# Kernel tuning notes

Measured on AMD Instinct MI355X. Metric: run time of the kernel, lower is better.

## Reference

```python
import jax, jax.numpy as jnp
import numpy as np
import math

HEAD_DEPTH = 16
CLIP = 10.0
NEG_INF = 1.0e10
# combined scale: (1/sqrt(head_depth)) * log_50(400)
SCALE = (math.log(400.0) / math.log(50.0)) / math.sqrt(HEAD_DEPTH)


def setup_inputs() -> dict:
    key = jax.random.key(0)
    kq, kk, kv, km = jax.random.split(key, 4)
    B, H, S, D = 4, 8, 2048, HEAD_DEPTH
    Q = jax.random.normal(kq, (B, H, S, D), dtype=jnp.float32)
    K = jax.random.normal(kk, (B, H, S, D), dtype=jnp.float32)
    V = jax.random.normal(kv, (B, H, S, D), dtype=jnp.float32)
    # mask: (B, n_nodes, 1) bool; True -> masked (logit set to -inf)
    mask = jax.random.randint(km, (B, S, 1), 0, 2) == 1
    return {"Q": Q, "K": K, "V": V, "mask": mask}


def reference(Q, K, V, mask):
    # logits: (B, H, q_seq, k_seq)
    logits = jnp.einsum("bhqd,bhkd->bhqk", Q, K) * SCALE
    logits = CLIP * jnp.tanh(logits)  # tanh clip
    # mask[:, None, None, :, 0] -> (B, 1, 1, k_seq), True gets -inf
    m = mask[:, None, None, :, 0]
    logits = jnp.where(m, -NEG_INF, logits)
    probs = jax.nn.softmax(logits, axis=-1)
    return jnp.einsum("bhqk,bhkd->bhqd", probs, V)
```

## Files before the change

kernel.cpp:

```cpp
#include <hip/hip_runtime.h>


typedef __fp16 h2 __attribute__((ext_vector_type(2)));
typedef __fp16 h4 __attribute__((ext_vector_type(4)));
typedef float  f4 __attribute__((ext_vector_type(4)));
typedef unsigned short us4 __attribute__((ext_vector_type(4)));

#define SEQ 2048

__device__ __forceinline__ float fast_exp2(float x) {
#if __has_builtin(__builtin_amdgcn_exp2f)
    return __builtin_amdgcn_exp2f(x);
#else
    return exp2f(x);
#endif
}

__device__ __forceinline__ float dot2acc(h2 a, float accv) {
#if __has_builtin(__builtin_amdgcn_fdot2)
    const h2 one = {(__fp16)1.0f, (__fp16)1.0f};
    return __builtin_amdgcn_fdot2(a, one, accv, false);
#else
    return accv + (float)a[0] + (float)a[1];
#endif
}

__global__ __launch_bounds__(512, 8) void attn_fused(
    const float* __restrict__ Qp, const float* __restrict__ Kp,
    const float* __restrict__ Vp, const int* __restrict__ maskp,
    float* __restrict__ out)
{
    __shared__ __align__(16) _Float16 Kbuf[2][4096];
    __shared__ __align__(16) _Float16 Vbuf[2][4096];
    __shared__ __align__(16) unsigned short idx16[SEQ];
    __shared__ int wsum[8];

    const int bid  = blockIdx.x;
    const int bh   = bid >> 5;
    const int qblk = bid & 31;
    const int b    = bh >> 3;
    const int tid  = threadIdx.x;
    const int wave = tid >> 6;
    const int lane = tid & 63;
    const int qt   = wave & 3;
    const int kg   = wave >> 2;
    const int c    = lane & 15;
    const int g    = lane >> 4;

    const size_t base  = (size_t)bh * (SEQ * 16);
    const int    qbase = qblk * 64 + qt * 16;
    const float  c1 = 1.1047809f;
    const float  c2 = -28.8539008f;

    h4 qfrag;
    {
        f4 qv = *(const f4*)(Qp + base + (size_t)(qbase + c) * 16 + 4 * g);
        h2 lo = __builtin_amdgcn_cvt_pkrtz(c1 * qv[0], c1 * qv[1]);
        h2 hi = __builtin_amdgcn_cvt_pkrtz(c1 * qv[2], c1 * qv[3]);
        qfrag[0] = lo[0]; qfrag[1] = lo[1]; qfrag[2] = hi[0]; qfrag[3] = hi[1];
    }

    int4 mv = *(const int4*)(maskp + (size_t)b * SEQ + tid * 4);
    const int k0 = (mv.x == 0), k1 = (mv.y == 0),
              k2 = (mv.z == 0), k3 = (mv.w == 0);
    const int cnt4 = k0 + k1 + k2 + k3;
    int inc = cnt4;
    #pragma unroll
    for (int off = 1; off < 64; off <<= 1) {
        int v = __shfl_up(inc, off);
        if (lane >= off) inc += v;
    }
    *(us4*)&idx16[tid * 4] = (us4){0, 0, 0, 0};
    if (lane == 63) wsum[wave] = inc;
    __syncthreads();
    int tot = 0, wpre = 0;
    #pragma unroll
    for (int w = 0; w < 8; ++w) {
        int s = wsum[w];
        if (w < wave) wpre += s;
        tot += s;
    }
    int pos = wpre + inc - cnt4;
    if (k0) idx16[pos++] = (unsigned short)(tid * 4 + 0);
    if (k1) idx16[pos++] = (unsigned short)(tid * 4 + 1);
    if (k2) idx16[pos++] = (unsigned short)(tid * 4 + 2);
    if (k3) idx16[pos++] = (unsigned short)(tid * 4 + 3);
    __syncthreads();

    int nr = (tot + 255) >> 8;
    if (nr == 0) nr = 1;

    const int u  = tid & 31;
    const int tt = tid >> 5;
    const int gc = u & 15;
    const int gh = u >> 4;

    const float* Kb = Kp + base;
    const float* Vb = Vp + base;

    const int fs0 = (tt * 64 + u)      * 4;
    const int fs1 = (tt * 64 + u + 32) * 4;

    f4 kA, kB;
    float vA0, vA1, vA2, vA3, vB0, vB1, vB2, vB3;

    {
        us4 ra = *(const us4*)&idx16[tt * 16 + 4 * gh];
        us4 rb = *(const us4*)&idx16[tt * 16 + 4 * gh + 8];
        const int krow = idx16[tt * 16 + gc];
        const float* kr = Kb + (size_t)krow * 16;
        f4 ka_ = *(const f4*)(kr + 4 * gh);
        f4 kb_ = *(const f4*)(kr + 4 * gh + 8);
        float a0 = Vb[(size_t)ra[0] * 16 + gc];
        float a1 = Vb[(size_t)ra[1] * 16 + gc];
        float a2 = Vb[(size_t)ra[2] * 16 + gc];
        float a3 = Vb[(size_t)ra[3] * 16 + gc];
        float b0 = Vb[(size_t)rb[0] * 16 + gc];
        float b1 = Vb[(size_t)rb[1] * 16 + gc];
        float b2 = Vb[(size_t)rb[2] * 16 + gc];
        float b3 = Vb[(size_t)rb[3] * 16 + gc];
        h2 x0 = __builtin_amdgcn_cvt_pkrtz(ka_[0], ka_[1]);
        h2 x1 = __builtin_amdgcn_cvt_pkrtz(ka_[2], ka_[3]);
        h4 kha; kha[0] = x0[0]; kha[1] = x0[1]; kha[2] = x1[0]; kha[3] = x1[1];
        *(h4*)&Kbuf[0][fs0] = kha;
        h2 y0 = __builtin_amdgcn_cvt_pkrtz(kb_[0], kb_[1]);
        h2 y1 = __builtin_amdgcn_cvt_pkrtz(kb_[2], kb_[3]);
        h4 khb; khb[0] = y0[0]; khb[1] = y0[1]; khb[2] = y1[0]; khb[3] = y1[1];
        *(h4*)&Kbuf[0][fs1] = khb;
        h2 p0 = __builtin_amdgcn_cvt_pkrtz(a0, a1);
        h2 p1 = __builtin_amdgcn_cvt_pkrtz(a2, a3);
        h4 vha; vha[0] = p0[0]; vha[1] = p0[1]; vha[2] = p1[0]; vha[3] = p1[1];
        *(h4*)&Vbuf[0][fs0] = vha;
        h2 q0 = __builtin_amdgcn_cvt_pkrtz(b0, b1);
        h2 q1 = __builtin_amdgcn_cvt_pkrtz(b2, b3);
        h4 vhb; vhb[0] = q0[0]; vhb[1] = q0[1]; vhb[2] = q1[0]; vhb[3] = q1[1];
        *(h4*)&Vbuf[0][fs1] = vhb;
    }
    {
        const int r1 = (nr > 1) ? 1 : 0;
        const int ib = r1 * 256 + tt * 16;
        us4 ra = *(const us4*)&idx16[ib + 4 * gh];
        us4 rb = *(const us4*)&idx16[ib + 4 * gh + 8];
        const int krow = idx16[ib + gc];
        const float* kr = Kb + (size_t)krow * 16;
        kA = *(const f4*)(kr + 4 * gh);
        kB = *(const f4*)(kr + 4 * gh + 8);
        vA0 = Vb[(size_t)ra[0] * 16 + gc];
        vA1 = Vb[(size_t)ra[1] * 16 + gc];
        vA2 = Vb[(size_t)ra[2] * 16 + gc];
        vA3 = Vb[(size_t)ra[3] * 16 + gc];
        vB0 = Vb[(size_t)rb[0] * 16 + gc];
        vB1 = Vb[(size_t)rb[1] * 16 + gc];
        vB2 = Vb[(size_t)rb[2] * 16 + gc];
        vB3 = Vb[(size_t)rb[3] * 16 + gc];
    }
    __syncthreads();

    f4 acc = {0.f, 0.f, 0.f, 0.f};
    float dsum = 0.f;

    for (int r = 0; r < nr; ++r) {
        const int cb = r & 1, nb = cb ^ 1;
        if (r + 1 < nr) {
            h2 x0 = __builtin_amdgcn_cvt_pkrtz(kA[0], kA[1]);
            h2 x1 = __builtin_amdgcn_cvt_pkrtz(kA[2], kA[3]);
            h4 kha; kha[0] = x0[0]; kha[1] = x0[1]; kha[2] = x1[0]; kha[3] = x1[1];
            *(h4*)&Kbuf[nb][fs0] = kha;
            h2 y0 = __builtin_amdgcn_cvt_pkrtz(kB[0], kB[1]);
            h2 y1 = __builtin_amdgcn_cvt_pkrtz(kB[2], kB[3]);
            h4 khb; khb[0] = y0[0]; khb[1] = y0[1]; khb[2] = y1[0]; khb[3] = y1[1];
            *(h4*)&Kbuf[nb][fs1] = khb;
            h2 p0 = __builtin_amdgcn_cvt_pkrtz(vA0, vA1);
            h2 p1 = __builtin_amdgcn_cvt_pkrtz(vA2, vA3);
            h4 vha; vha[0] = p0[0]; vha[1] = p0[1]; vha[2] = p1[0]; vha[3] = p1[1];
            *(h4*)&Vbuf[nb][fs0] = vha;
            h2 q0 = __builtin_amdgcn_cvt_pkrtz(vB0, vB1);
            h2 q1 = __builtin_amdgcn_cvt_pkrtz(vB2, vB3);
            h4 vhb; vhb[0] = q0[0]; vhb[1] = q0[1]; vhb[2] = q1[0]; vhb[3] = q1[1];
            *(h4*)&Vbuf[nb][fs1] = vhb;
        }
        if (r + 2 < nr) {
            const int ib = (r + 2) * 256 + tt * 16;
            us4 ra = *(const us4*)&idx16[ib + 4 * gh];
            us4 rb = *(const us4*)&idx16[ib + 4 * gh + 8];
            const int krow = idx16[ib + gc];
            const float* kr = Kb + (size_t)krow * 16;
            kA = *(const f4*)(kr + 4 * gh);
            kB = *(const f4*)(kr + 4 * gh + 8);
            vA0 = Vb[(size_t)ra[0] * 16 + gc];
            vA1 = Vb[(size_t)ra[1] * 16 + gc];
            vA2 = Vb[(size_t)ra[2] * 16 + gc];
            vA3 = Vb[(size_t)ra[3] * 16 + gc];
            vB0 = Vb[(size_t)rb[0] * 16 + gc];
            vB1 = Vb[(size_t)rb[1] * 16 + gc];
            vB2 = Vb[(size_t)rb[2] * 16 + gc];
            vB3 = Vb[(size_t)rb[3] * 16 + gc];
        }

        const _Float16* Kc = &Kbuf[cb][kg * 2048];
        const _Float16* Vc = &Vbuf[cb][kg * 2048];
        const int lim = tot - r * 256 - kg * 128 - 4 * g;

        #pragma unroll
        for (int t = 0; t < 8; ++t) {
            h4 afrag = *(const h4*)(Kc + t * 256 + lane * 4);
            f4 s = __builtin_amdgcn_mfma_f32_16x16x16f16(
                afrag, qfrag, (f4){0.f, 0.f, 0.f, 0.f}, 0, 0, 0);

            float p[4];
            #pragma unroll
            for (int i = 0; i < 4; ++i) {
                float tv = fast_exp2(s[i]);
                float w  = __builtin_amdgcn_rcpf(1.0f + tv);
                float bsel = (t * 16 + i < lim) ? 0.0f : -1.0e30f;
                p[i] = fast_exp2(__builtin_fmaf(c2, w, bsel));
            }
            h2 plo = __builtin_amdgcn_cvt_pkrtz(p[0], p[1]);
            h2 phi = __builtin_amdgcn_cvt_pkrtz(p[2], p[3]);
            dsum = dot2acc(plo, dsum);
            dsum = dot2acc(phi, dsum);
            h4 pf; pf[0] = plo[0]; pf[1] = plo[1]; pf[2] = phi[0]; pf[3] = phi[1];

            h4 vfrag = *(const h4*)(Vc + t * 256 + lane * 4);
            acc = __builtin_amdgcn_mfma_f32_16x16x16f16(pf, vfrag, acc, 0, 0, 0);
        }
        __syncthreads();
    }

    dsum += __shfl_xor(dsum, 16);
    dsum += __shfl_xor(dsum, 32);

    float* ex = (float*)&Kbuf[0][0];
    const int slot = (qt * 64 + lane) * 5;
    if (kg == 1) {
        ex[slot + 0] = acc[0]; ex[slot + 1] = acc[1];
        ex[slot + 2] = acc[2]; ex[slot + 3] = acc[3];
        ex[slot + 4] = dsum;
    }
    __syncthreads();
    if (kg == 0) {
        const float dT = dsum + ex[slot + 4];
        #pragma unroll
        for (int i = 0; i < 4; ++i) {
            const float denom = __shfl(dT, 4 * g + i);
            out[base + (size_t)(qbase + 4 * g + i) * 16 + c] =
                (acc[i] + ex[slot + i]) / denom;
        }
    }
}

extern "C" void kernel_launch(void* const* d_in, const int* in_sizes, int n_in,
                              void* d_out, int out_size, void* d_ws, size_t ws_size,
                              hipStream_t stream) {
    const float* Q    = (const float*)d_in[0];
    const float* K    = (const float*)d_in[1];
    const float* V    = (const float*)d_in[2];
    const int*   mask = (const int*)d_in[3];
    float* out = (float*)d_out;
    attn_fused<<<dim3(1024), dim3(512), 0, stream>>>(Q, K, V, mask, out);
}
```

Baseline: 94.12 us.

## Process two query tiles per wave, halve grid, skip masking on full chunks

Each wave now computes two 16-row query tiles against the same shared K/V fragments. This halves the number of blocks and the total gather/convert work for compacted K/V per query. Full chunks drop the per-element mask-select computation, and the final partial chunk iterates only over the tiles that are populated. The trade-offs are more registers per thread (launch bounds relaxed to 4), fewer blocks in flight on the device, and a longer serial dependency chain per wave.

```diff
diff --git a/kernel.cpp b/kernel.cpp
--- a/kernel.cpp
+++ b/kernel.cpp
@@ -25,7 +25,23 @@
 #endif
 }
 
-__global__ __launch_bounds__(512, 8) void attn_fused(
+__device__ __forceinline__ h4 prob4(f4 s, f4 bsel, float c2, float& dsum) {
+    float p[4];
+    #pragma unroll
+    for (int i = 0; i < 4; ++i) {
+        float tv = fast_exp2(s[i]);
+        float w  = __builtin_amdgcn_rcpf(1.0f + tv);
+        p[i] = fast_exp2(__builtin_fmaf(c2, w, bsel[i]));
+    }
+    h2 plo = __builtin_amdgcn_cvt_pkrtz(p[0], p[1]);
+    h2 phi = __builtin_amdgcn_cvt_pkrtz(p[2], p[3]);
+    dsum = dot2acc(plo, dsum);
+    dsum = dot2acc(phi, dsum);
+    h4 pf; pf[0] = plo[0]; pf[1] = plo[1]; pf[2] = phi[0]; pf[3] = phi[1];
+    return pf;
+}
+
+__global__ __launch_bounds__(512, 4) void attn_fused(
     const float* __restrict__ Qp, const float* __restrict__ Kp,
     const float* __restrict__ Vp, const int* __restrict__ maskp,
     float* __restrict__ out)
@@ -36,8 +52,8 @@
     __shared__ int wsum[8];
 
     const int bid  = blockIdx.x;
-    const int bh   = bid >> 5;
-    const int qblk = bid & 31;
+    const int bh   = bid >> 4;
+    const int qblk = bid & 15;
     const int b    = bh >> 3;
     const int tid  = threadIdx.x;
     const int wave = tid >> 6;
@@ -48,16 +64,21 @@
     const int g    = lane >> 4;
 
     const size_t base  = (size_t)bh * (SEQ * 16);
-    const int    qbase = qblk * 64 + qt * 16;
+    const int    qb0   = qblk * 128 + qt * 16;
+    const int    qb1   = qb0 + 64;
     const float  c1 = 1.1047809f;
     const float  c2 = -28.8539008f;
 
-    h4 qfrag;
+    h4 qfrag0, qfrag1;
     {
-        f4 qv = *(const f4*)(Qp + base + (size_t)(qbase + c) * 16 + 4 * g);
+        f4 qv = *(const f4*)(Qp + base + (size_t)(qb0 + c) * 16 + 4 * g);
         h2 lo = __builtin_amdgcn_cvt_pkrtz(c1 * qv[0], c1 * qv[1]);
         h2 hi = __builtin_amdgcn_cvt_pkrtz(c1 * qv[2], c1 * qv[3]);
-        qfrag[0] = lo[0]; qfrag[1] = lo[1]; qfrag[2] = hi[0]; qfrag[3] = hi[1];
+        qfrag0[0] = lo[0]; qfrag0[1] = lo[1]; qfrag0[2] = hi[0]; qfrag0[3] = hi[1];
+        f4 qw = *(const f4*)(Qp + base + (size_t)(qb1 + c) * 16 + 4 * g);
+        h2 l2 = __builtin_amdgcn_cvt_pkrtz(c1 * qw[0], c1 * qw[1]);
+        h2 h2_ = __builtin_amdgcn_cvt_pkrtz(c1 * qw[2], c1 * qw[3]);
+        qfrag1[0] = l2[0]; qfrag1[1] = l2[1]; qfrag1[2] = h2_[0]; qfrag1[3] = h2_[1];
     }
 
     int4 mv = *(const int4*)(maskp + (size_t)b * SEQ + tid * 4);
@@ -156,8 +177,8 @@
     }
     __syncthreads();
 
-    f4 acc = {0.f, 0.f, 0.f, 0.f};
-    float dsum = 0.f;
+    f4 acc0 = {0.f, 0.f, 0.f, 0.f}, acc1 = {0.f, 0.f, 0.f, 0.f};
+    float dsum0 = 0.f, dsum1 = 0.f;
 
     for (int r = 0; r < nr; ++r) {
         const int cb = r & 1, nb = cb ^ 1;
@@ -199,52 +220,75 @@
 
         const _Float16* Kc = &Kbuf[cb][kg * 2048];
         const _Float16* Vc = &Vbuf[cb][kg * 2048];
-        const int lim = tot - r * 256 - kg * 128 - 4 * g;
-
-        #pragma unroll
-        for (int t = 0; t < 8; ++t) {
-            h4 afrag = *(const h4*)(Kc + t * 256 + lane * 4);
-            f4 s = __builtin_amdgcn_mfma_f32_16x16x16f16(
-                afrag, qfrag, (f4){0.f, 0.f, 0.f, 0.f}, 0, 0, 0);
-
-            float p[4];
+
+        if (r + 1 < nr) {
+            const f4 z = {0.f, 0.f, 0.f, 0.f};
             #pragma unroll
-            for (int i = 0; i < 4; ++i) {
-                float tv = fast_exp2(s[i]);
-                float w  = __builtin_amdgcn_rcpf(1.0f + tv);
-                float bsel = (t * 16 + i < lim) ? 0.0f : -1.0e30f;
-                p[i] = fast_exp2(__builtin_fmaf(c2, w, bsel));
+            for (int t = 0; t < 8; ++t) {
+                h4 afrag = *(const h4*)(Kc + t * 256 + lane * 4);
+                f4 s0 = __builtin_amdgcn_mfma_f32_16x16x16f16(
+                    afrag, qfrag0, (f4){0.f, 0.f, 0.f, 0.f}, 0, 0, 0);
+                f4 s1 = __builtin_amdgcn_mfma_f32_16x16x16f16(
+                    afrag, qfrag1, (f4){0.f, 0.f, 0.f, 0.f}, 0, 0, 0);
+                h4 pf0 = prob4(s0, z, c2, dsum0);
+                h4 pf1 = prob4(s1, z, c2, dsum1);
+                h4 vfrag = *(const h4*)(Vc + t * 256 + lane * 4);
+                acc0 = __builtin_amdgcn_mfma_f32_16x16x16f16(pf0, vfrag, acc0, 0, 0, 0);
+                acc1 = __builtin_amdgcn_mfma_f32_16x16x16f16(pf1, vfrag, acc1, 0, 0, 0);
             }
-            h2 plo = __builtin_amdgcn_cvt_pkrtz(p[0], p[1]);
-            h2 phi = __builtin_amdgcn_cvt_pkrtz(p[2], p[3]);
-            dsum = dot2acc(plo, dsum);
-            dsum = dot2acc(phi, dsum);
-            h4 pf; pf[0] = plo[0]; pf[1] = plo[1]; pf[2] = phi[0]; pf[3] = phi[1];
-
-            h4 vfrag = *(const h4*)(Vc + t * 256 + lane * 4);
-            acc = __builtin_amdgcn_mfma_f32_16x16x16f16(pf, vfrag, acc, 0, 0, 0);
+        } else {
+            const int rem  = tot - r * 256 - kg * 128;
+            int tcnt = (rem <= 0) ? 0 : ((rem + 15) >> 4);
+            if (tcnt > 8) tcnt = 8;
+            const int lim = rem - 4 * g;
+            for (int t = 0; t < tcnt; ++t) {
+                h4 afrag = *(const h4*)(Kc + t * 256 + lane * 4);
+                f4 s0 = __builtin_amdgcn_mfma_f32_16x16x16f16(
+                    afrag, qfrag0, (f4){0.f, 0.f, 0.f, 0.f}, 0, 0, 0);
+                f4 s1 = __builtin_amdgcn_mfma_f32_16x16x16f16(
+                    afrag, qfrag1, (f4){0.f, 0.f, 0.f, 0.f}, 0, 0, 0);
+                f4 bsel;
+                #pragma unroll
+                for (int i = 0; i < 4; ++i)
+                    bsel[i] = (t * 16 + i < lim) ? 0.0f : -1.0e30f;
+                h4 pf0 = prob4(s0, bsel, c2, dsum0);
+                h4 pf1 = prob4(s1, bsel, c2, dsum1);
+                h4 vfrag = *(const h4*)(Vc + t * 256 + lane * 4);
+                acc0 = __builtin_amdgcn_mfma_f32_16x16x16f16(pf0, vfrag, acc0, 0, 0, 0);
+                acc1 = __builtin_amdgcn_mfma_f32_16x16x16f16(pf1, vfrag, acc1, 0, 0, 0);
+            }
         }
         __syncthreads();
     }
 
-    dsum += __shfl_xor(dsum, 16);
-    dsum += __shfl_xor(dsum, 32);
+    dsum0 += __shfl_xor(dsum0, 16);
+    dsum0 += __shfl_xor(dsum0, 32);
+    dsum1 += __shfl_xor(dsum1, 16);
+    dsum1 += __shfl_xor(dsum1, 32);
 
     float* ex = (float*)&Kbuf[0][0];
-    const int slot = (qt * 64 + lane) * 5;
+    const int slot0 = ((qt)     * 64 + lane) * 5;
+    const int slot1 = ((qt + 4) * 64 + lane) * 5;
     if (kg == 1) {
-        ex[slot + 0] = acc[0]; ex[slot + 1] = acc[1];
-        ex[slot + 2] = acc[2]; ex[slot + 3] = acc[3];
-        ex[slot + 4] = dsum;
+        ex[slot0 + 0] = acc0[0]; ex[slot0 + 1] = acc0[1];
+        ex[slot0 + 2] = acc0[2]; ex[slot0 + 3] = acc0[3];
+        ex[slot0 + 4] = dsum0;
+        ex[slot1 + 0] = acc1[0]; ex[slot1 + 1] = acc1[1];
+        ex[slot1 + 2] = acc1[2]; ex[slot1 + 3] = acc1[3];
+        ex[slot1 + 4] = dsum1;
     }
     __syncthreads();
     if (kg == 0) {
-        const float dT = dsum + ex[slot + 4];
+        const float dT0 = dsum0 + ex[slot0 + 4];
+        const float dT1 = dsum1 + ex[slot1 + 4];
         #pragma unroll
         for (int i = 0; i < 4; ++i) {
-            const float denom = __shfl(dT, 4 * g + i);
-            out[base + (size_t)(qbase + 4 * g + i) * 16 + c] =
-                (acc[i] + ex[slot + i]) / denom;
+            const float den0 = __shfl(dT0, 4 * g + i);
+            out[base + (size_t)(qb0 + 4 * g + i) * 16 + c] =
+                (acc0[i] + ex[slot0 + i]) / den0;
+            const float den1 = __shfl(dT1, 4 * g + i);
+            out[base + (size_t)(qb1 + 4 * g + i) * 16 + c] =
+                (acc1[i] + ex[slot1 + i]) / den1;
         }
     }
 }
@@ -257,5 +301,5 @@
     const float* V    = (const float*)d_in[2];
     const int*   mask = (const int*)d_in[3];
     float* out = (float*)d_out;
-    attn_fused<<<dim3(1024), dim3(512), 0, stream>>>(Q, K, V, mask, out);
-}
+    attn_fused<<<dim3(512), dim3(512), 0, stream>>>(Q, K, V, mask, out);
+}
```

After: 91.03 us, median of 2. -3.3%, faster.

## Process four query tiles per block to reuse staged K/V and skip masked tail

Applied to the files above, without the earlier changes.

Each block now handles 256 queries (four 16-row Q fragments per wave) instead of 64, so every gathered and fp16-converted K/V tile in shared memory is reused across four times as many queries and the grid shrinks from 1024 to 256 blocks. The last round is split into its own path that only iterates over tiles holding valid (unmasked) keys and applies the mask bias there, while full rounds skip the mask select. This cuts global gather traffic and conversion work per query, at the cost of more registers per thread, a lower occupancy hint, and only 256 blocks, which may leave compute units underused.

```diff
diff --git a/kernel.cpp b/kernel.cpp
--- a/kernel.cpp
+++ b/kernel.cpp
@@ -25,7 +25,23 @@
 #endif
 }
 
-__global__ __launch_bounds__(512, 8) void attn_fused(
+__device__ __forceinline__ h4 prob4(f4 s, f4 bsel, float c2, float& dsum) {
+    float p[4];
+    #pragma unroll
+    for (int i = 0; i < 4; ++i) {
+        float tv = fast_exp2(s[i]);
+        float w  = __builtin_amdgcn_rcpf(1.0f + tv);
+        p[i] = fast_exp2(__builtin_fmaf(c2, w, bsel[i]));
+    }
+    h2 plo = __builtin_amdgcn_cvt_pkrtz(p[0], p[1]);
+    h2 phi = __builtin_amdgcn_cvt_pkrtz(p[2], p[3]);
+    dsum = dot2acc(plo, dsum);
+    dsum = dot2acc(phi, dsum);
+    h4 pf; pf[0] = plo[0]; pf[1] = plo[1]; pf[2] = phi[0]; pf[3] = phi[1];
+    return pf;
+}
+
+__global__ __launch_bounds__(512, 2) void attn_fused(
     const float* __restrict__ Qp, const float* __restrict__ Kp,
     const float* __restrict__ Vp, const int* __restrict__ maskp,
     float* __restrict__ out)
@@ -36,8 +52,8 @@
     __shared__ int wsum[8];
 
     const int bid  = blockIdx.x;
-    const int bh   = bid >> 5;
-    const int qblk = bid & 31;
+    const int bh   = bid >> 3;
+    const int qblk = bid & 7;
     const int b    = bh >> 3;
     const int tid  = threadIdx.x;
     const int wave = tid >> 6;
@@ -47,17 +63,19 @@
     const int c    = lane & 15;
     const int g    = lane >> 4;
 
-    const size_t base  = (size_t)bh * (SEQ * 16);
-    const int    qbase = qblk * 64 + qt * 16;
+    const size_t base = (size_t)bh * (SEQ * 16);
     const float  c1 = 1.1047809f;
     const float  c2 = -28.8539008f;
 
-    h4 qfrag;
-    {
-        f4 qv = *(const f4*)(Qp + base + (size_t)(qbase + c) * 16 + 4 * g);
+    h4 qfrag[4];
+    #pragma unroll
+    for (int j = 0; j < 4; ++j) {
+        const int qb = qblk * 256 + qt * 16 + j * 64;
+        f4 qv = *(const f4*)(Qp + base + (size_t)(qb + c) * 16 + 4 * g);
         h2 lo = __builtin_amdgcn_cvt_pkrtz(c1 * qv[0], c1 * qv[1]);
         h2 hi = __builtin_amdgcn_cvt_pkrtz(c1 * qv[2], c1 * qv[3]);
-        qfrag[0] = lo[0]; qfrag[1] = lo[1]; qfrag[2] = hi[0]; qfrag[3] = hi[1];
+        qfrag[j][0] = lo[0]; qfrag[j][1] = lo[1];
+        qfrag[j][2] = hi[0]; qfrag[j][3] = hi[1];
     }
 
     int4 mv = *(const int4*)(maskp + (size_t)b * SEQ + tid * 4);
@@ -156,8 +174,10 @@
     }
     __syncthreads();
 
-    f4 acc = {0.f, 0.f, 0.f, 0.f};
-    float dsum = 0.f;
+    f4 acc[4];
+    #pragma unroll
+    for (int j = 0; j < 4; ++j) acc[j] = (f4){0.f, 0.f, 0.f, 0.f};
+    float dsum[4] = {0.f, 0.f, 0.f, 0.f};
 
     for (int r = 0; r < nr; ++r) {
         const int cb = r & 1, nb = cb ^ 1;
@@ -199,52 +219,81 @@
 
         const _Float16* Kc = &Kbuf[cb][kg * 2048];
         const _Float16* Vc = &Vbuf[cb][kg * 2048];
-        const int lim = tot - r * 256 - kg * 128 - 4 * g;
-
+
+        if (r + 1 < nr) {
+            const f4 z = {0.f, 0.f, 0.f, 0.f};
+            #pragma unroll
+            for (int t = 0; t < 8; ++t) {
+                h4 afrag = *(const h4*)(Kc + t * 256 + lane * 4);
+                h4 vfrag = *(const h4*)(Vc + t * 256 + lane * 4);
+                #pragma unroll
+                for (int j = 0; j < 4; ++j) {
+                    f4 s = __builtin_amdgcn_mfma_f32_16x16x16f16(
+                        afrag, qfrag[j], (f4){0.f, 0.f, 0.f, 0.f}, 0, 0, 0);
+                    h4 pf = prob4(s, z, c2, dsum[j]);
+                    acc[j] = __builtin_amdgcn_mfma_f32_16x16x16f16(
+                        pf, vfrag, acc[j], 0, 0, 0);
+                }
+            }
+        } else {
+            const int rem  = tot - r * 256 - kg * 128;
+            int tcnt = (rem <= 0) ? 0 : ((rem + 15) >> 4);
+            if (tcnt > 8) tcnt = 8;
+            const int lim = rem - 4 * g;
+            for (int t = 0; t < tcnt; ++t) {
+                h4 afrag = *(const h4*)(Kc + t * 256 + lane * 4);
+                h4 vfrag = *(const h4*)(Vc + t * 256 + lane * 4);
+                f4 bsel;
+                #pragma unroll
+                for (int i = 0; i < 4; ++i)
+                    bsel[i] = (t * 16 + i < lim) ? 0.0f : -1.0e30f;
+                #pragma unroll
+                for (int j = 0; j < 4; ++j) {
+                    f4 s = __builtin_amdgcn_mfma_f32_16x16x16f16(
+                        afrag, qfrag[j], (f4){0.f, 0.f, 0.f, 0.f}, 0, 0, 0);
+                    h4 pf = prob4(s, bsel, c2, dsum[j]);
+                    acc[j] = __builtin_amdgcn_mfma_f32_16x16x16f16(
+                        pf, vfrag, acc[j], 0, 0, 0);
+                }
+            }
+        }
+        __syncthreads();
+    }
+
+    #pragma unroll
+    for (int j = 0; j < 4; ++j) {
+        dsum[j] += __shfl_xor(dsum[j], 16);
+        dsum[j] += __shfl_xor(dsum[j], 32);
+    }
+
+    float* exA = (float*)&Kbuf[0][0];
+    float* exB = (float*)&Vbuf[0][0];
+    int slot[4];
+    #pragma unroll
+    for (int j = 0; j < 4; ++j)
+        slot[j] = (((j & 1) * 4 + qt) * 64 + lane) * 5;
+    if (kg == 1) {
         #pragma unroll
-        for (int t = 0; t < 8; ++t) {
-            h4 afrag = *(const h4*)(Kc + t * 256 + lane * 4);
-            f4 s = __builtin_amdgcn_mfma_f32_16x16x16f16(
-                afrag, qfrag, (f4){0.f, 0.f, 0.f, 0.f}, 0, 0, 0);
-
-            float p[4];
+        for (int j = 0; j < 4; ++j) {
+            float* ex = (j < 2) ? exA : exB;
+            ex[slot[j] + 0] = acc[j][0]; ex[slot[j] + 1] = acc[j][1];
+            ex[slot[j] + 2] = acc[j][2]; ex[slot[j] + 3] = acc[j][3];
+            ex[slot[j] + 4] = dsum[j];
+        }
+    }
+    __syncthreads();
+    if (kg == 0) {
+        #pragma unroll
+        for (int j = 0; j < 4; ++j) {
+            float* ex = (j < 2) ? exA : exB;
+            const int qb = qblk * 256 + qt * 16 + j * 64;
+            const float dT = dsum[j] + ex[slot[j] + 4];
             #pragma unroll
             for (int i = 0; i < 4; ++i) {
-                float tv = fast_exp2(s[i]);
-                float w  = __builtin_amdgcn_rcpf(1.0f + tv);
-                float bsel = (t * 16 + i < lim) ? 0.0f : -1.0e30f;
-                p[i] = fast_exp2(__builtin_fmaf(c2, w, bsel));
+                const float denom = __shfl(dT, 4 * g + i);
+                out[base + (size_t)(qb + 4 * g + i) * 16 + c] =
+                    (acc[j][i] + ex[slot[j] + i]) / denom;
             }
-            h2 plo = __builtin_amdgcn_cvt_pkrtz(p[0], p[1]);
-            h2 phi = __builtin_amdgcn_cvt_pkrtz(p[2], p[3]);
-            dsum = dot2acc(plo, dsum);
-            dsum = dot2acc(phi, dsum);
-            h4 pf; pf[0] = plo[0]; pf[1] = plo[1]; pf[2] = phi[0]; pf[3] = phi[1];
-
-            h4 vfrag = *(const h4*)(Vc + t * 256 + lane * 4);
-            acc = __builtin_amdgcn_mfma_f32_16x16x16f16(pf, vfrag, acc, 0, 0, 0);
-        }
-        __syncthreads();
-    }
-
-    dsum += __shfl_xor(dsum, 16);
-    dsum += __shfl_xor(dsum, 32);
-
-    float* ex = (float*)&Kbuf[0][0];
-    const int slot = (qt * 64 + lane) * 5;
-    if (kg == 1) {
-        ex[slot + 0] = acc[0]; ex[slot + 1] = acc[1];
-        ex[slot + 2] = acc[2]; ex[slot + 3] = acc[3];
-        ex[slot + 4] = dsum;
-    }
-    __syncthreads();
-    if (kg == 0) {
-        const float dT = dsum + ex[slot + 4];
-        #pragma unroll
-        for (int i = 0; i < 4; ++i) {
-            const float denom = __shfl(dT, 4 * g + i);
-            out[base + (size_t)(qbase + 4 * g + i) * 16 + c] =
-                (acc[i] + ex[slot + i]) / denom;
         }
     }
 }
@@ -257,5 +306,5 @@
     const float* V    = (const float*)d_in[2];
     const int*   mask = (const int*)d_in[3];
     float* out = (float*)d_out;
-    attn_fused<<<dim3(1024), dim3(512), 0, stream>>>(Q, K, V, mask, out);
-}
+    attn_fused<<<dim3(256), dim3(512), 0, stream>>>(Q, K, V, mask, out);
+}
```

Measured after the change: 93.09 us. No clear change (-1.1%).
